# Kernel tuning notes

Hardware: AMD Instinct MI355X
Metric: run time of the kernel (lower is better)

Reference implementation:

```python
import jax, jax.numpy as jnp
import numpy as np
import math

N_HEAD = 16

def setup_inputs() -> dict:
    key = jax.random.key(0)
    ks = jax.random.split(key, 8)
    B, S, P, NX = 4, 1024, 128, 1024
    return {
        "x": jax.random.normal(ks[0], (B, S, NX), jnp.float32),
        "M": jax.random.normal(ks[1], (B, P, NX), jnp.float32),
        "Mmask": jnp.ones((B, P), jnp.float32),
        "attention_mask": jnp.zeros((B, 1, 1, S), jnp.float32),
        "W_attn": jax.random.normal(ks[2], (NX, 3 * NX), jnp.float32) * 0.02,
        "b_attn": jnp.zeros((3 * NX,), jnp.float32),
        "W_mem": jax.random.normal(ks[3], (NX, 2 * NX), jnp.float32) * 0.02,
        "b_mem": jnp.zeros((2 * NX,), jnp.float32),
        "W_proj": jax.random.normal(ks[4], (NX, NX), jnp.float32) * 0.02,
        "b_proj": jnp.zeros((NX,), jnp.float32),
    }

def _split_heads(t, H):
    B, T, NX = t.shape
    return t.reshape(B, T, H, NX // H).transpose(0, 2, 1, 3)  # [B,H,T,dh]

def reference(x, M, Mmask, attention_mask, W_attn, b_attn, W_mem, b_mem, W_proj, b_proj):
    B, S, NX = x.shape
    H = N_HEAD
    dh = NX // H
    P = M.shape[1]

    # fused QKV projection (Conv1D == x @ W + b)
    qkv = x @ W_attn + b_attn
    q, k, v = jnp.split(qkv, 3, axis=2)

    # memory K/V projection, prepended along the key/value sequence axis
    ekv = M @ W_mem + b_mem
    ek, ev = jnp.split(ekv, 2, axis=2)
    key = jnp.concatenate([ek, k], axis=1)   # [B, P+S, NX]
    value = jnp.concatenate([ev, v], axis=1)

    qh = _split_heads(q, H)      # [B,H,S,dh]
    kh = _split_heads(key, H)    # [B,H,P+S,dh]
    vh = _split_heads(value, H)  # [B,H,P+S,dh]

    w = jnp.einsum('bhsd,bhtd->bhst', qh, kh) / math.sqrt(dh)  # [B,H,S,P+S]

    # causal bias over the self part, all-ones over the memory part
    causal = jnp.tril(jnp.ones((S, S), w.dtype))
    b = jnp.concatenate([jnp.ones((S, P), w.dtype), causal], axis=1)[None, None]  # [1,1,S,P+S]
    w = w * b - 10000.0 * (1.0 - b)

    # additive attention mask: memory-mask bias concatenated before token mask
    mem_bias = (1.0 - Mmask)[:, None, None, :] * -10000.0  # [B,1,1,P]
    am = jnp.concatenate([mem_bias, jnp.broadcast_to(attention_mask, (B, 1, 1, S))], axis=3)
    w = w + am

    w = jax.nn.softmax(w, axis=-1)
    a = jnp.einsum('bhst,bhtd->bhsd', w, vh)                  # [B,H,S,dh]
    a = a.transpose(0, 2, 1, 3).reshape(B, S, NX)             # merge heads
    return a @ W_proj + b_proj
```

## Files before the change

kernel.cpp:

```cpp
#include <hip/hip_runtime.h>
#include <hip/hip_bf16.h>


typedef __attribute__((ext_vector_type(8))) short bf16x8;
typedef __attribute__((ext_vector_type(4))) float f32x4;

#define MFMA16(a, b, c) __builtin_amdgcn_mfma_f32_16x16x32_bf16((a), (b), (c), 0, 0, 0)

#define GLOAD_LDS16(g, l)                                                  \
    __builtin_amdgcn_global_load_lds(                                      \
        (const __attribute__((address_space(1))) void*)(const void*)(g),   \
        (__attribute__((address_space(3))) void*)(void*)(l), 16, 0, 0)

static __device__ __forceinline__ unsigned short f2bf(float f) {
    union { float f; unsigned int u; } v; v.f = f;
    unsigned int u = v.u;
    return (unsigned short)((u + 0x7fffu + ((u >> 16) & 1u)) >> 16);
}

__global__ void cvt_all(const float* __restrict__ x, const float* __restrict__ Mem,
                        unsigned short* __restrict__ x_bf, unsigned short* __restrict__ M_bf) {
    int i = blockIdx.x * 256 + threadIdx.x;
    if (i < 1048576) {
        float4 v = ((const float4*)x)[i];
        ushort4 o; o.x = f2bf(v.x); o.y = f2bf(v.y); o.z = f2bf(v.z); o.w = f2bf(v.w);
        ((ushort4*)x_bf)[i] = o;
    } else {
        int j = i - 1048576;
        float4 v = ((const float4*)Mem)[j];
        ushort4 o; o.x = f2bf(v.x); o.y = f2bf(v.y); o.z = f2bf(v.z); o.w = f2bf(v.w);
        ((ushort4*)M_bf)[j] = o;
    }
}

static __device__ __forceinline__ void transpose_body(const float* __restrict__ W,
                                                      unsigned short* __restrict__ Wt,
                                                      int K, int N, int bx, int by,
                                                      float (*tile)[33]) {
    int n0 = bx * 32, k0 = by * 32;
    int tx = threadIdx.x & 31, ty = threadIdx.x >> 5;
    #pragma unroll
    for (int r = ty; r < 32; r += 8) tile[r][tx] = W[(size_t)(k0 + r) * N + n0 + tx];
    __syncthreads();
    #pragma unroll
    for (int r = ty; r < 32; r += 8) Wt[(size_t)(n0 + r) * K + k0 + tx] = f2bf(tile[tx][r]);
}

__global__ void prep_weights(const float* __restrict__ W_attn, const float* __restrict__ W_mem,
                             const float* __restrict__ W_proj, unsigned short* __restrict__ Wat,
                             unsigned short* __restrict__ Wmt, unsigned short* __restrict__ Wpt,
                             const float* __restrict__ Mmask, const float* __restrict__ amask,
                             float* __restrict__ biasT) {
    __shared__ float tile[32][33];
    int bid = blockIdx.x;
    if (bid < 3072) {
        transpose_body(W_attn, Wat, 1024, 3072, bid % 96, bid / 96, tile);
    } else if (bid < 5120) {
        int t = bid - 3072; transpose_body(W_mem, Wmt, 1024, 2048, t % 64, t / 64, tile);
    } else if (bid < 6144) {
        int t = bid - 5120; transpose_body(W_proj, Wpt, 1024, 1024, t % 32, t / 32, tile);
    } else {
        int i = (bid - 6144) * 256 + threadIdx.x;
        if (i < 4 * 1152) {
            int b = i / 1152, t = i % 1152;
            float v = (t < 128) ? (Mmask[b * 128 + t] - 1.f) * 10000.f
                                : amask[b * 1024 + t - 128];
            biasT[i] = v * 1.4426950408889634f;
        }
    }
}

__global__ __launch_bounds__(256) void build_kv(const unsigned short* __restrict__ QKV,
                                                const unsigned short* __restrict__ EKV,
                                                unsigned short* __restrict__ Kc,
                                                unsigned short* __restrict__ Vt) {
    __shared__ unsigned short vt[64][72];
    const int tid = threadIdx.x;
    const int blk = blockIdx.x;
    const int tc = blk % 18, bh = blk / 18;
    const int h = bh & 15, b = bh >> 4;
    const int row = tid >> 2, c = (tid & 3) * 16;
    const int tg = tc * 64 + row;
    const unsigned short* src;
    if (tg < 128) src = EKV + (size_t)(b * 128 + tg) * 2048 + h * 64 + c;
    else          src = QKV + (size_t)(b * 1024 + tg - 128) * 3072 + 1024 + h * 64 + c;
    bf16x8 ka = *(const bf16x8*)src;
    bf16x8 kb = *(const bf16x8*)(src + 8);
    bf16x8 va = *(const bf16x8*)(src + 1024);
    bf16x8 vb = *(const bf16x8*)(src + 1032);
    unsigned short* kd = Kc + (size_t)bh * 73728 + (size_t)tg * 64 + c;
    *(bf16x8*)kd = ka;
    *(bf16x8*)(kd + 8) = kb;
    *(bf16x8*)&vt[row][c] = va;
    *(bf16x8*)&vt[row][c + 8] = vb;
    __syncthreads();
    bf16x8 o0, o1;
    #pragma unroll
    for (int j = 0; j < 8; j++) { o0[j] = vt[c + j][row]; o1[j] = vt[c + 8 + j][row]; }
    unsigned short* vd = Vt + (size_t)bh * 73728 + (size_t)row * 1152 + tc * 64 + c;
    *(bf16x8*)vd = o0;
    *(bf16x8*)(vd + 8) = o1;
}

template <int TN, int STORE_BF16>
static __device__ __forceinline__ void gemm_body(const unsigned short* __restrict__ A,
                                                 const unsigned short* __restrict__ Bt,
                                                 const float* __restrict__ bias,
                                                 void* __restrict__ C, int bm, int bn,
                                                 int N, int K,
                                                 unsigned short* As, unsigned short* Bs) {
    constexpr int NJ = TN / 32;
    constexpr int NCH = 8 + TN / 16;
    const int tid = threadIdx.x;
    const int lane = tid & 63, wave = tid >> 6;
    const int quad = lane >> 4, l16 = lane & 15;
    const int wm = (wave & 1) * 64, wn = (wave >> 1) * (TN / 2);
    const int crow = lane >> 2, ccol = (lane & 3) * 8;
    const unsigned short* Abase = A + (size_t)(bm * 128 + crow) * K + ccol;
    const unsigned short* Bbase = Bt + (size_t)(bn * TN + crow) * K + ccol;

    f32x4 acc[4][NJ] = {};
    for (int k0 = 0; k0 < K; k0 += 32) {
        __syncthreads();
        #pragma unroll
        for (int cc = 0; cc < NCH / 4; cc++) {
            const int c = wave * (NCH / 4) + cc;
            if (c < 8) GLOAD_LDS16(Abase + (size_t)(c * 16) * K + k0, &As[c * 512]);
            else       GLOAD_LDS16(Bbase + (size_t)((c - 8) * 16) * K + k0, &Bs[(c - 8) * 512]);
        }
        __syncthreads();
        bf16x8 af[4], bf[NJ];
        #pragma unroll
        for (int i = 0; i < 4; i++) af[i] = *(const bf16x8*)&As[(wm + i * 16 + l16) * 32 + quad * 8];
        #pragma unroll
        for (int j = 0; j < NJ; j++) bf[j] = *(const bf16x8*)&Bs[(wn + j * 16 + l16) * 32 + quad * 8];
        #pragma unroll
        for (int i = 0; i < 4; i++)
            #pragma unroll
            for (int j = 0; j < NJ; j++)
                acc[i][j] = MFMA16(af[i], bf[j], acc[i][j]);
    }
    float bj[NJ];
    #pragma unroll
    for (int j = 0; j < NJ; j++) bj[j] = bias[bn * TN + wn + j * 16 + l16];
    #pragma unroll
    for (int i = 0; i < 4; i++) {
        const int row = bm * 128 + wm + i * 16 + quad * 4;
        #pragma unroll
        for (int j = 0; j < NJ; j++) {
            const int col = bn * TN + wn + j * 16 + l16;
            #pragma unroll
            for (int r = 0; r < 4; r++) {
                float v = acc[i][j][r] + bj[j];
                if (STORE_BF16)
                    ((unsigned short*)C)[(size_t)(row + r) * N + col] = f2bf(v);
                else
                    ((float*)C)[(size_t)(row + r) * N + col] = v;
            }
        }
    }
}

__global__ __launch_bounds__(256) void gemm_qkv_ekv(const unsigned short* __restrict__ x_bf,
                                                    const unsigned short* __restrict__ Wat,
                                                    const float* __restrict__ b_attn,
                                                    unsigned short* __restrict__ QKV,
                                                    const unsigned short* __restrict__ M_bf,
                                                    const unsigned short* __restrict__ Wmt,
                                                    const float* __restrict__ b_mem,
                                                    unsigned short* __restrict__ EKV) {
    __shared__ unsigned short As[128 * 32];
    __shared__ unsigned short Bs[128 * 32];
    const int bid = blockIdx.x;
    if (bid < 768)
        gemm_body<128, 1>(x_bf, Wat, b_attn, QKV, bid & 31, bid >> 5, 3072, 1024, As, Bs);
    else {
        const int t = bid - 768;
        gemm_body<128, 1>(M_bf, Wmt, b_mem, EKV, t & 3, t >> 2, 2048, 1024, As, Bs);
    }
}

__global__ __launch_bounds__(256) void gemm_proj(const unsigned short* __restrict__ Abuf,
                                                 const unsigned short* __restrict__ Wpt,
                                                 const float* __restrict__ b_proj,
                                                 float* __restrict__ out) {
    __shared__ unsigned short As[128 * 32];
    __shared__ unsigned short Bs[64 * 32];
    const int bid = blockIdx.x;
    gemm_body<64, 0>(Abuf, Wpt, b_proj, out, bid & 31, bid >> 5, 1024, 1024, As, Bs);
}

__global__ __launch_bounds__(256) void attn_kernel(const unsigned short* __restrict__ QKV,
                                                   const unsigned short* __restrict__ Kc,
                                                   const unsigned short* __restrict__ Vt,
                                                   const float* __restrict__ biasT,
                                                   unsigned short* __restrict__ Aout) {
    __shared__ unsigned short Ks[2 * 64 * 32];
    __shared__ unsigned short Vs[2 * 64 * 32];
    __shared__ unsigned short Ps[4][16 * 72];
    const int tid = threadIdx.x;
    const int lane = tid & 63, wave = tid >> 6;
    const int quad = lane >> 4, l16 = lane & 15;
    const int blk = blockIdx.x;
    const int xcd = blk & 7, idx = blk >> 3;
    const int bh = xcd * 8 + (idx >> 4);
    const int qg = 15 - (idx & 15);
    const int h = bh & 15, b = bh >> 4;
    const int qrow0 = qg * 64;
    const int qrow_w = qrow0 + wave * 16;

    bf16x8 qf[2];
    #pragma unroll
    for (int k2 = 0; k2 < 2; k2++)
        qf[k2] = *(const bf16x8*)(QKV + (size_t)(b * 1024 + qrow_w + l16) * 3072 +
                                  h * 64 + k2 * 32 + quad * 8);

    const unsigned short* Kb = Kc + (size_t)bh * 73728;
    const unsigned short* Vb = Vt + (size_t)bh * 73728;
    const float* bias_b = biasT + b * 1152;

    const int srow = lane >> 2;
    const int sc8 = (lane & 3) * 8;

    bf16x8 ones;
    #pragma unroll
    for (int j = 0; j < 8; j++) ones[j] = (short)0x3F80;

    f32x4 o[4] = {};
    f32x4 oden = {};
    const int tmax = min(1152, qrow0 + 192);

    for (int t0 = 0; t0 < tmax; t0 += 64) {
        __syncthreads();
        #pragma unroll
        for (int cc = 0; cc < 4; cc++) {
            const int c = wave * 4 + cc;
            if (c < 8) {
                const int kk = c & 1, rch = c >> 1;
                GLOAD_LDS16(Kb + (size_t)(t0 + rch * 16 + srow) * 64 + kk * 32 + sc8,
                            &Ks[kk * 2048 + rch * 512]);
            } else {
                const int c2 = c - 8, tk = c2 & 1, dch = c2 >> 1;
                GLOAD_LDS16(Vb + (size_t)(dch * 16 + srow) * 1152 + t0 + tk * 32 + sc8,
                            &Vs[tk * 2048 + dch * 512]);
            }
        }
        __syncthreads();
        if (t0 <= qrow_w + 143) {
            const bool nomask = (t0 + 63 <= 128 + qrow_w);
            float4 bt[4];
            #pragma unroll
            for (int tn = 0; tn < 4; tn++)
                bt[tn] = *(const float4*)(bias_b + t0 + tn * 16 + quad * 4);
            const int sg = qrow_w + l16;
            #pragma unroll
            for (int tn = 0; tn < 4; tn++) {
                bf16x8 kf0 = *(const bf16x8*)&Ks[0 * 2048 + (tn * 16 + l16) * 32 + quad * 8];
                bf16x8 kf1 = *(const bf16x8*)&Ks[1 * 2048 + (tn * 16 + l16) * 32 + quad * 8];
                f32x4 st = {};
                st = MFMA16(kf0, qf[0], st);
                st = MFMA16(kf1, qf[1], st);
                float p[4];
                #pragma unroll
                for (int r = 0; r < 4; r++) {
                    float e = __builtin_amdgcn_exp2f(st[r] * 0.18033688011112042f + bt[tn][r]);
                    if (!nomask) {
                        const int tg = t0 + tn * 16 + quad * 4 + r;
                        e = (tg < 128 || tg - 128 <= sg) ? e : 0.f;
                    }
                    p[r] = e;
                }
                union { ushort4 u; __hip_bfloat162 h2[2]; } pk;
                pk.h2[0] = __float22bfloat162_rn(float2{p[0], p[1]});
                pk.h2[1] = __float22bfloat162_rn(float2{p[2], p[3]});
                *(ushort4*)&Ps[wave][l16 * 72 + tn * 16 + quad * 4] = pk.u;
            }
            #pragma unroll
            for (int tk = 0; tk < 2; tk++) {
                bf16x8 pf = *(const bf16x8*)&Ps[wave][l16 * 72 + tk * 32 + quad * 8];
                oden = MFMA16(pf, ones, oden);
                #pragma unroll
                for (int dn = 0; dn < 4; dn++) {
                    bf16x8 vf = *(const bf16x8*)&Vs[tk * 2048 + (dn * 16 + l16) * 32 + quad * 8];
                    o[dn] = MFMA16(pf, vf, o[dn]);
                }
            }
        }
    }

    #pragma unroll
    for (int r = 0; r < 4; r++) {
        const float inv = 1.f / oden[r];
        const size_t orow = (size_t)(b * 1024 + qrow_w + quad * 4 + r) * 1024 + h * 64;
        #pragma unroll
        for (int dn = 0; dn < 4; dn++)
            Aout[orow + dn * 16 + l16] = f2bf(o[dn][r] * inv);
    }
}

extern "C" void kernel_launch(void* const* d_in, const int* in_sizes, int n_in,
                              void* d_out, int out_size, void* d_ws, size_t ws_size,
                              hipStream_t stream) {
    const float* x      = (const float*)d_in[0];
    const float* Mem    = (const float*)d_in[1];
    const float* Mmask  = (const float*)d_in[2];
    const float* amask  = (const float*)d_in[3];
    const float* W_attn = (const float*)d_in[4];
    const float* b_attn = (const float*)d_in[5];
    const float* W_mem  = (const float*)d_in[6];
    const float* b_mem  = (const float*)d_in[7];
    const float* W_proj = (const float*)d_in[8];
    const float* b_proj = (const float*)d_in[9];
    float* out = (float*)d_out;

    char* ws = (char*)d_ws;
    unsigned short* x_bf  = (unsigned short*)ws;  ws += (size_t)4096 * 1024 * 2;
    unsigned short* M_bf  = (unsigned short*)ws;  ws += (size_t)512 * 1024 * 2;
    unsigned short* Wat   = (unsigned short*)ws;  ws += (size_t)3072 * 1024 * 2;
    unsigned short* Wmt   = (unsigned short*)ws;  ws += (size_t)2048 * 1024 * 2;
    unsigned short* Wpt   = (unsigned short*)ws;  ws += (size_t)1024 * 1024 * 2;
    unsigned short* QKV   = (unsigned short*)ws;  ws += (size_t)4096 * 3072 * 2;
    unsigned short* EKV   = (unsigned short*)ws;  ws += (size_t)512 * 2048 * 2;
    unsigned short* Abuf  = (unsigned short*)ws;  ws += (size_t)4096 * 1024 * 2;
    unsigned short* Kc    = (unsigned short*)ws;  ws += (size_t)64 * 1152 * 64 * 2;
    unsigned short* Vt    = (unsigned short*)ws;  ws += (size_t)64 * 64 * 1152 * 2;
    float*          biasT = (float*)ws;           ws += (size_t)4 * 1152 * 4;

    cvt_all<<<4608, 256, 0, stream>>>(x, Mem, x_bf, M_bf);
    prep_weights<<<6163, 256, 0, stream>>>(W_attn, W_mem, W_proj, Wat, Wmt, Wpt,
                                           Mmask, amask, biasT);
    gemm_qkv_ekv<<<832, 256, 0, stream>>>(x_bf, Wat, b_attn, QKV, M_bf, Wmt, b_mem, EKV);
    build_kv<<<1152, 256, 0, stream>>>(QKV, EKV, Kc, Vt);
    attn_kernel<<<1024, 256, 0, stream>>>(QKV, Kc, Vt, biasT, Abuf);
    gemm_proj<<<512, 256, 0, stream>>>(Abuf, Wpt, b_proj, out);
}
```

Measured before the change: 227.5 us.

## Fuse K/V relayout into projection GEMM epilogue and merge prep kernels

Merges the activation-conversion and weight-prep kernels into one launch. The QKV/memory-KV GEMM now writes Q to its own buffer and scatters K and transposed V straight into the attention layouts from its epilogue, with the V transpose staged through LDS. This removes the build_kv kernel and the round trip through the full QKV/EKV intermediates. The memory-KV GEMM now uses smaller 64x64 tiles so it gets more blocks. The K epilogue stores are scattered 2-byte writes, and the extra LDS staging and __syncthreads add some epilogue cost.

```diff
diff --git a/kernel.cpp b/kernel.cpp
--- a/kernel.cpp
+++ b/kernel.cpp
@@ -16,21 +16,6 @@
     union { float f; unsigned int u; } v; v.f = f;
     unsigned int u = v.u;
     return (unsigned short)((u + 0x7fffu + ((u >> 16) & 1u)) >> 16);
-}
-
-__global__ void cvt_all(const float* __restrict__ x, const float* __restrict__ Mem,
-                        unsigned short* __restrict__ x_bf, unsigned short* __restrict__ M_bf) {
-    int i = blockIdx.x * 256 + threadIdx.x;
-    if (i < 1048576) {
-        float4 v = ((const float4*)x)[i];
-        ushort4 o; o.x = f2bf(v.x); o.y = f2bf(v.y); o.z = f2bf(v.z); o.w = f2bf(v.w);
-        ((ushort4*)x_bf)[i] = o;
-    } else {
-        int j = i - 1048576;
-        float4 v = ((const float4*)Mem)[j];
-        ushort4 o; o.x = f2bf(v.x); o.y = f2bf(v.y); o.z = f2bf(v.z); o.w = f2bf(v.w);
-        ((ushort4*)M_bf)[j] = o;
-    }
 }
 
 static __device__ __forceinline__ void transpose_body(const float* __restrict__ W,
@@ -46,13 +31,30 @@
     for (int r = ty; r < 32; r += 8) Wt[(size_t)(n0 + r) * K + k0 + tx] = f2bf(tile[tx][r]);
 }
 
-__global__ void prep_weights(const float* __restrict__ W_attn, const float* __restrict__ W_mem,
-                             const float* __restrict__ W_proj, unsigned short* __restrict__ Wat,
-                             unsigned short* __restrict__ Wmt, unsigned short* __restrict__ Wpt,
-                             const float* __restrict__ Mmask, const float* __restrict__ amask,
-                             float* __restrict__ biasT) {
+__global__ void prep_all(const float* __restrict__ x, const float* __restrict__ Mem,
+                         unsigned short* __restrict__ x_bf, unsigned short* __restrict__ M_bf,
+                         const float* __restrict__ W_attn, const float* __restrict__ W_mem,
+                         const float* __restrict__ W_proj, unsigned short* __restrict__ Wat,
+                         unsigned short* __restrict__ Wmt, unsigned short* __restrict__ Wpt,
+                         const float* __restrict__ Mmask, const float* __restrict__ amask,
+                         float* __restrict__ biasT) {
     __shared__ float tile[32][33];
     int bid = blockIdx.x;
+    if (bid < 4608) {
+        int i = bid * 256 + threadIdx.x;
+        if (i < 1048576) {
+            float4 v = ((const float4*)x)[i];
+            ushort4 o; o.x = f2bf(v.x); o.y = f2bf(v.y); o.z = f2bf(v.z); o.w = f2bf(v.w);
+            ((ushort4*)x_bf)[i] = o;
+        } else {
+            int j = i - 1048576;
+            float4 v = ((const float4*)Mem)[j];
+            ushort4 o; o.x = f2bf(v.x); o.y = f2bf(v.y); o.z = f2bf(v.z); o.w = f2bf(v.w);
+            ((ushort4*)M_bf)[j] = o;
+        }
+        return;
+    }
+    bid -= 4608;
     if (bid < 3072) {
         transpose_body(W_attn, Wat, 1024, 3072, bid % 96, bid / 96, tile);
     } else if (bid < 5120) {
@@ -70,127 +72,163 @@
     }
 }
 
-__global__ __launch_bounds__(256) void build_kv(const unsigned short* __restrict__ QKV,
-                                                const unsigned short* __restrict__ EKV,
-                                                unsigned short* __restrict__ Kc,
-                                                unsigned short* __restrict__ Vt) {
-    __shared__ unsigned short vt[64][72];
-    const int tid = threadIdx.x;
-    const int blk = blockIdx.x;
-    const int tc = blk % 18, bh = blk / 18;
-    const int h = bh & 15, b = bh >> 4;
-    const int row = tid >> 2, c = (tid & 3) * 16;
-    const int tg = tc * 64 + row;
-    const unsigned short* src;
-    if (tg < 128) src = EKV + (size_t)(b * 128 + tg) * 2048 + h * 64 + c;
-    else          src = QKV + (size_t)(b * 1024 + tg - 128) * 3072 + 1024 + h * 64 + c;
-    bf16x8 ka = *(const bf16x8*)src;
-    bf16x8 kb = *(const bf16x8*)(src + 8);
-    bf16x8 va = *(const bf16x8*)(src + 1024);
-    bf16x8 vb = *(const bf16x8*)(src + 1032);
-    unsigned short* kd = Kc + (size_t)bh * 73728 + (size_t)tg * 64 + c;
-    *(bf16x8*)kd = ka;
-    *(bf16x8*)(kd + 8) = kb;
-    *(bf16x8*)&vt[row][c] = va;
-    *(bf16x8*)&vt[row][c + 8] = vb;
-    __syncthreads();
-    bf16x8 o0, o1;
-    #pragma unroll
-    for (int j = 0; j < 8; j++) { o0[j] = vt[c + j][row]; o1[j] = vt[c + 8 + j][row]; }
-    unsigned short* vd = Vt + (size_t)bh * 73728 + (size_t)row * 1152 + tc * 64 + c;
-    *(bf16x8*)vd = o0;
-    *(bf16x8*)(vd + 8) = o1;
-}
-
-template <int TN, int STORE_BF16>
-static __device__ __forceinline__ void gemm_body(const unsigned short* __restrict__ A,
-                                                 const unsigned short* __restrict__ Bt,
-                                                 const float* __restrict__ bias,
-                                                 void* __restrict__ C, int bm, int bn,
-                                                 int N, int K,
-                                                 unsigned short* As, unsigned short* Bs) {
-    constexpr int NJ = TN / 32;
-    constexpr int NCH = 8 + TN / 16;
+__global__ __launch_bounds__(256, 4) void gemm_fused(
+        const unsigned short* __restrict__ x_bf, const unsigned short* __restrict__ Wat,
+        const float* __restrict__ b_attn, const unsigned short* __restrict__ M_bf,
+        const unsigned short* __restrict__ Wmt, const float* __restrict__ b_mem,
+        unsigned short* __restrict__ Qbuf, unsigned short* __restrict__ Kc,
+        unsigned short* __restrict__ Vt) {
+    __shared__ char smem[34816];
+    unsigned short* As = (unsigned short*)smem;
+    unsigned short* Bs = (unsigned short*)(smem + 8192);
     const int tid = threadIdx.x;
     const int lane = tid & 63, wave = tid >> 6;
     const int quad = lane >> 4, l16 = lane & 15;
-    const int wm = (wave & 1) * 64, wn = (wave >> 1) * (TN / 2);
     const int crow = lane >> 2, ccol = (lane & 3) * 8;
-    const unsigned short* Abase = A + (size_t)(bm * 128 + crow) * K + ccol;
-    const unsigned short* Bbase = Bt + (size_t)(bn * TN + crow) * K + ccol;
-
-    f32x4 acc[4][NJ] = {};
-    for (int k0 = 0; k0 < K; k0 += 32) {
-        __syncthreads();
-        #pragma unroll
-        for (int cc = 0; cc < NCH / 4; cc++) {
-            const int c = wave * (NCH / 4) + cc;
-            if (c < 8) GLOAD_LDS16(Abase + (size_t)(c * 16) * K + k0, &As[c * 512]);
-            else       GLOAD_LDS16(Bbase + (size_t)((c - 8) * 16) * K + k0, &Bs[(c - 8) * 512]);
-        }
-        __syncthreads();
-        bf16x8 af[4], bf[NJ];
-        #pragma unroll
-        for (int i = 0; i < 4; i++) af[i] = *(const bf16x8*)&As[(wm + i * 16 + l16) * 32 + quad * 8];
-        #pragma unroll
-        for (int j = 0; j < NJ; j++) bf[j] = *(const bf16x8*)&Bs[(wn + j * 16 + l16) * 32 + quad * 8];
-        #pragma unroll
-        for (int i = 0; i < 4; i++)
-            #pragma unroll
-            for (int j = 0; j < NJ; j++)
-                acc[i][j] = MFMA16(af[i], bf[j], acc[i][j]);
-    }
-    float bj[NJ];
-    #pragma unroll
-    for (int j = 0; j < NJ; j++) bj[j] = bias[bn * TN + wn + j * 16 + l16];
-    #pragma unroll
-    for (int i = 0; i < 4; i++) {
-        const int row = bm * 128 + wm + i * 16 + quad * 4;
-        #pragma unroll
-        for (int j = 0; j < NJ; j++) {
-            const int col = bn * TN + wn + j * 16 + l16;
-            #pragma unroll
-            for (int r = 0; r < 4; r++) {
-                float v = acc[i][j][r] + bj[j];
-                if (STORE_BF16)
-                    ((unsigned short*)C)[(size_t)(row + r) * N + col] = f2bf(v);
-                else
-                    ((float*)C)[(size_t)(row + r) * N + col] = v;
-            }
-        }
-    }
-}
-
-__global__ __launch_bounds__(256) void gemm_qkv_ekv(const unsigned short* __restrict__ x_bf,
-                                                    const unsigned short* __restrict__ Wat,
-                                                    const float* __restrict__ b_attn,
-                                                    unsigned short* __restrict__ QKV,
-                                                    const unsigned short* __restrict__ M_bf,
-                                                    const unsigned short* __restrict__ Wmt,
-                                                    const float* __restrict__ b_mem,
-                                                    unsigned short* __restrict__ EKV) {
-    __shared__ unsigned short As[128 * 32];
-    __shared__ unsigned short Bs[128 * 32];
     const int bid = blockIdx.x;
-    if (bid < 768)
-        gemm_body<128, 1>(x_bf, Wat, b_attn, QKV, bid & 31, bid >> 5, 3072, 1024, As, Bs);
-    else {
+
+    if (bid < 768) {
+        const int bm = bid & 31, bn = bid >> 5;
+        const int wm = (wave & 1) * 64, wn = (wave >> 1) * 64;
+        const unsigned short* Abase = x_bf + (size_t)(bm * 128 + crow) * 1024 + ccol;
+        const unsigned short* Bbase = Wat + (size_t)(bn * 128 + crow) * 1024 + ccol;
+        f32x4 acc[4][4] = {};
+        for (int k0 = 0; k0 < 1024; k0 += 32) {
+            __syncthreads();
+            #pragma unroll
+            for (int cc = 0; cc < 4; cc++) {
+                const int c = wave * 4 + cc;
+                if (c < 8) GLOAD_LDS16(Abase + (size_t)(c * 16) * 1024 + k0, &As[c * 512]);
+                else       GLOAD_LDS16(Bbase + (size_t)((c - 8) * 16) * 1024 + k0, &Bs[(c - 8) * 512]);
+            }
+            __syncthreads();
+            bf16x8 af[4], bf[4];
+            #pragma unroll
+            for (int i = 0; i < 4; i++) af[i] = *(const bf16x8*)&As[(wm + i * 16 + l16) * 32 + quad * 8];
+            #pragma unroll
+            for (int j = 0; j < 4; j++) bf[j] = *(const bf16x8*)&Bs[(wn + j * 16 + l16) * 32 + quad * 8];
+            #pragma unroll
+            for (int i = 0; i < 4; i++)
+                #pragma unroll
+                for (int j = 0; j < 4; j++)
+                    acc[i][j] = MFMA16(af[i], bf[j], acc[i][j]);
+        }
+        float bj[4];
+        #pragma unroll
+        for (int j = 0; j < 4; j++) bj[j] = b_attn[bn * 128 + wn + j * 16 + l16];
+        __syncthreads();
+        if (bn < 8) {
+            #pragma unroll
+            for (int i = 0; i < 4; i++) {
+                const int row = bm * 128 + wm + i * 16 + quad * 4;
+                #pragma unroll
+                for (int j = 0; j < 4; j++) {
+                    const int col = bn * 128 + wn + j * 16 + l16;
+                    #pragma unroll
+                    for (int r = 0; r < 4; r++)
+                        Qbuf[(size_t)(row + r) * 1024 + col] = f2bf(acc[i][j][r] + bj[j]);
+                }
+            }
+        } else if (bn < 16) {
+            #pragma unroll
+            for (int i = 0; i < 4; i++) {
+                const int row = bm * 128 + wm + i * 16 + quad * 4;
+                const int b = row >> 10, s = row & 1023;
+                #pragma unroll
+                for (int j = 0; j < 4; j++) {
+                    const int c = bn * 128 + wn + j * 16 + l16 - 1024;
+                    unsigned short* kd = Kc + (size_t)((b << 4) | (c >> 6)) * 73728 +
+                                         (size_t)(s + 128) * 64 + (c & 63);
+                    #pragma unroll
+                    for (int r = 0; r < 4; r++) kd[(size_t)r * 64] = f2bf(acc[i][j][r] + bj[j]);
+                }
+            }
+        } else {
+            unsigned short* Tw = (unsigned short*)smem + wave * 4352;
+            #pragma unroll
+            for (int i = 0; i < 4; i++)
+                #pragma unroll
+                for (int j = 0; j < 4; j++)
+                    #pragma unroll
+                    for (int r = 0; r < 4; r++)
+                        Tw[(j * 16 + l16) * 68 + i * 16 + quad * 4 + r] = f2bf(acc[i][j][r] + bj[j]);
+            const int vb = (bn - 16) * 128 + wn;
+            const int h = vb >> 6;
+            const int b = bm >> 3, s0 = (bm * 128 + wm) & 1023;
+            unsigned short* vd = Vt + (size_t)((b << 4) | h) * 73728 +
+                                 (size_t)lane * 1152 + 128 + s0;
+            #pragma unroll
+            for (int ch = 0; ch < 8; ch++)
+                *(bf16x8*)(vd + ch * 8) = *(const bf16x8*)&Tw[lane * 68 + ch * 8];
+        }
+    } else {
         const int t = bid - 768;
-        gemm_body<128, 1>(M_bf, Wmt, b_mem, EKV, t & 3, t >> 2, 2048, 1024, As, Bs);
-    }
-}
-
-__global__ __launch_bounds__(256) void gemm_proj(const unsigned short* __restrict__ Abuf,
-                                                 const unsigned short* __restrict__ Wpt,
-                                                 const float* __restrict__ b_proj,
-                                                 float* __restrict__ out) {
-    __shared__ unsigned short As[128 * 32];
-    __shared__ unsigned short Bs[64 * 32];
-    const int bid = blockIdx.x;
-    gemm_body<64, 0>(Abuf, Wpt, b_proj, out, bid & 31, bid >> 5, 1024, 1024, As, Bs);
-}
-
-__global__ __launch_bounds__(256) void attn_kernel(const unsigned short* __restrict__ QKV,
+        const int bm = t >> 5, bn = t & 31;
+        const int wm = (wave & 1) * 32, wn = (wave >> 1) * 32;
+        const unsigned short* Abase = M_bf + (size_t)(bm * 64 + crow) * 1024 + ccol;
+        const unsigned short* Bbase = Wmt + (size_t)(bn * 64 + crow) * 1024 + ccol;
+        f32x4 acc[2][2] = {};
+        for (int k0 = 0; k0 < 1024; k0 += 32) {
+            __syncthreads();
+            #pragma unroll
+            for (int cc = 0; cc < 2; cc++) {
+                const int c = wave * 2 + cc;
+                if (c < 4) GLOAD_LDS16(Abase + (size_t)(c * 16) * 1024 + k0, &As[c * 512]);
+                else       GLOAD_LDS16(Bbase + (size_t)((c - 4) * 16) * 1024 + k0, &Bs[(c - 4) * 512]);
+            }
+            __syncthreads();
+            bf16x8 af[2], bf[2];
+            #pragma unroll
+            for (int i = 0; i < 2; i++) af[i] = *(const bf16x8*)&As[(wm + i * 16 + l16) * 32 + quad * 8];
+            #pragma unroll
+            for (int j = 0; j < 2; j++) bf[j] = *(const bf16x8*)&Bs[(wn + j * 16 + l16) * 32 + quad * 8];
+            #pragma unroll
+            for (int i = 0; i < 2; i++)
+                #pragma unroll
+                for (int j = 0; j < 2; j++)
+                    acc[i][j] = MFMA16(af[i], bf[j], acc[i][j]);
+        }
+        float bj[2];
+        #pragma unroll
+        for (int j = 0; j < 2; j++) bj[j] = b_mem[bn * 64 + wn + j * 16 + l16];
+        __syncthreads();
+        if (bn < 16) {
+            #pragma unroll
+            for (int i = 0; i < 2; i++) {
+                const int row = bm * 64 + wm + i * 16 + quad * 4;
+                const int b = row >> 7, p = row & 127;
+                #pragma unroll
+                for (int j = 0; j < 2; j++) {
+                    const int c = bn * 64 + wn + j * 16 + l16;
+                    unsigned short* kd = Kc + (size_t)((b << 4) | (c >> 6)) * 73728 +
+                                         (size_t)p * 64 + (c & 63);
+                    #pragma unroll
+                    for (int r = 0; r < 4; r++) kd[(size_t)r * 64] = f2bf(acc[i][j][r] + bj[j]);
+                }
+            }
+        } else {
+            unsigned short* Tw = (unsigned short*)smem + wave * 1152;
+            #pragma unroll
+            for (int i = 0; i < 2; i++)
+                #pragma unroll
+                for (int j = 0; j < 2; j++)
+                    #pragma unroll
+                    for (int r = 0; r < 4; r++)
+                        Tw[(j * 16 + l16) * 36 + i * 16 + quad * 4 + r] = f2bf(acc[i][j][r] + bj[j]);
+            const int vb = bn * 64 + wn - 1024;
+            const int h = vb >> 6, d0 = vb & 63;
+            const int b = (bm * 64 + wm) >> 7, p0 = (bm * 64 + wm) & 127;
+            const int lc = lane >> 1, half = lane & 1;
+            unsigned short* vd = Vt + (size_t)((b << 4) | h) * 73728 +
+                                 (size_t)(d0 + lc) * 1152 + p0 + half * 16;
+            #pragma unroll
+            for (int ch = 0; ch < 2; ch++)
+                *(bf16x8*)(vd + ch * 8) = *(const bf16x8*)&Tw[lc * 36 + half * 16 + ch * 8];
+        }
+    }
+}
+
+__global__ __launch_bounds__(256) void attn_kernel(const unsigned short* __restrict__ Qbuf,
                                                    const unsigned short* __restrict__ Kc,
                                                    const unsigned short* __restrict__ Vt,
                                                    const float* __restrict__ biasT,
@@ -212,7 +250,7 @@
     bf16x8 qf[2];
     #pragma unroll
     for (int k2 = 0; k2 < 2; k2++)
-        qf[k2] = *(const bf16x8*)(QKV + (size_t)(b * 1024 + qrow_w + l16) * 3072 +
+        qf[k2] = *(const bf16x8*)(Qbuf + (size_t)(b * 1024 + qrow_w + l16) * 1024 +
                                   h * 64 + k2 * 32 + quad * 8);
 
     const unsigned short* Kb = Kc + (size_t)bh * 73728;
@@ -295,6 +333,58 @@
         #pragma unroll
         for (int dn = 0; dn < 4; dn++)
             Aout[orow + dn * 16 + l16] = f2bf(o[dn][r] * inv);
+    }
+}
+
+__global__ __launch_bounds__(256) void gemm_proj(const unsigned short* __restrict__ Abuf,
+                                                 const unsigned short* __restrict__ Wpt,
+                                                 const float* __restrict__ b_proj,
+                                                 float* __restrict__ out) {
+    __shared__ unsigned short As[128 * 32];
+    __shared__ unsigned short Bs[64 * 32];
+    const int tid = threadIdx.x;
+    const int lane = tid & 63, wave = tid >> 6;
+    const int quad = lane >> 4, l16 = lane & 15;
+    const int wm = (wave & 1) * 64, wn = (wave >> 1) * 32;
+    const int bm = blockIdx.x & 31, bn = blockIdx.x >> 5;
+    const int crow = lane >> 2, ccol = (lane & 3) * 8;
+    const unsigned short* Abase = Abuf + (size_t)(bm * 128 + crow) * 1024 + ccol;
+    const unsigned short* Bbase = Wpt + (size_t)(bn * 64 + crow) * 1024 + ccol;
+
+    f32x4 acc[4][2] = {};
+    for (int k0 = 0; k0 < 1024; k0 += 32) {
+        __syncthreads();
+        #pragma unroll
+        for (int cc = 0; cc < 3; cc++) {
+            const int c = wave * 3 + cc;
+            if (c < 8) GLOAD_LDS16(Abase + (size_t)(c * 16) * 1024 + k0, &As[c * 512]);
+            else if (c < 12) GLOAD_LDS16(Bbase + (size_t)((c - 8) * 16) * 1024 + k0, &Bs[(c - 8) * 512]);
+        }
+        __syncthreads();
+        bf16x8 af[4], bf[2];
+        #pragma unroll
+        for (int i = 0; i < 4; i++) af[i] = *(const bf16x8*)&As[(wm + i * 16 + l16) * 32 + quad * 8];
+        #pragma unroll
+        for (int j = 0; j < 2; j++) bf[j] = *(const bf16x8*)&Bs[(wn + j * 16 + l16) * 32 + quad * 8];
+        #pragma unroll
+        for (int i = 0; i < 4; i++)
+            #pragma unroll
+            for (int j = 0; j < 2; j++)
+                acc[i][j] = MFMA16(af[i], bf[j], acc[i][j]);
+    }
+    float bj[2];
+    #pragma unroll
+    for (int j = 0; j < 2; j++) bj[j] = b_proj[bn * 64 + wn + j * 16 + l16];
+    #pragma unroll
+    for (int i = 0; i < 4; i++) {
+        const int row = bm * 128 + wm + i * 16 + quad * 4;
+        #pragma unroll
+        for (int j = 0; j < 2; j++) {
+            const int col = bn * 64 + wn + j * 16 + l16;
+            #pragma unroll
+            for (int r = 0; r < 4; r++)
+                out[(size_t)(row + r) * 1024 + col] = acc[i][j][r] + bj[j];
+        }
     }
 }
 
@@ -319,18 +409,16 @@
     unsigned short* Wat   = (unsigned short*)ws;  ws += (size_t)3072 * 1024 * 2;
     unsigned short* Wmt   = (unsigned short*)ws;  ws += (size_t)2048 * 1024 * 2;
     unsigned short* Wpt   = (unsigned short*)ws;  ws += (size_t)1024 * 1024 * 2;
-    unsigned short* QKV   = (unsigned short*)ws;  ws += (size_t)4096 * 3072 * 2;
-    unsigned short* EKV   = (unsigned short*)ws;  ws += (size_t)512 * 2048 * 2;
+    unsigned short* Qbuf  = (unsigned short*)ws;  ws += (size_t)4096 * 1024 * 2;
     unsigned short* Abuf  = (unsigned short*)ws;  ws += (size_t)4096 * 1024 * 2;
     unsigned short* Kc    = (unsigned short*)ws;  ws += (size_t)64 * 1152 * 64 * 2;
     unsigned short* Vt    = (unsigned short*)ws;  ws += (size_t)64 * 64 * 1152 * 2;
     float*          biasT = (float*)ws;           ws += (size_t)4 * 1152 * 4;
 
-    cvt_all<<<4608, 256, 0, stream>>>(x, Mem, x_bf, M_bf);
-    prep_weights<<<6163, 256, 0, stream>>>(W_attn, W_mem, W_proj, Wat, Wmt, Wpt,
-                                           Mmask, amask, biasT);
-    gemm_qkv_ekv<<<832, 256, 0, stream>>>(x_bf, Wat, b_attn, QKV, M_bf, Wmt, b_mem, EKV);
-    build_kv<<<1152, 256, 0, stream>>>(QKV, EKV, Kc, Vt);
-    attn_kernel<<<1024, 256, 0, stream>>>(QKV, Kc, Vt, biasT, Abuf);
+    prep_all<<<10771, 256, 0, stream>>>(x, Mem, x_bf, M_bf, W_attn, W_mem, W_proj,
+                                        Wat, Wmt, Wpt, Mmask, amask, biasT);
+    gemm_fused<<<1024, 256, 0, stream>>>(x_bf, Wat, b_attn, M_bf, Wmt, b_mem,
+                                         Qbuf, Kc, Vt);
+    attn_kernel<<<1024, 256, 0, stream>>>(Qbuf, Kc, Vt, biasT, Abuf);
     gemm_proj<<<512, 256, 0, stream>>>(Abuf, Wpt, b_proj, out);
 }
```

After: 209.4 us. 1.09x faster.
